# Kernel tuning notes

Hardware: AMD Instinct MI355X
Metric: run time of the kernel (lower is better)

## Reference

```python
import jax, jax.numpy as jnp
import numpy as np

N_DOMAIN = 8
EPS = 1e-05
NUM_FEATURES = 1024
BATCH = 65536


def setup_inputs() -> dict:
    key = jax.random.key(0)
    k1, k2 = jax.random.split(key)
    x = jax.random.normal(k1, (BATCH, NUM_FEATURES), dtype=jnp.float32)
    y = jax.random.randint(k2, (BATCH,), 0, N_DOMAIN, dtype=jnp.int64)
    gamma = jnp.ones((1, NUM_FEATURES), dtype=jnp.float32)
    beta = jnp.zeros((1, NUM_FEATURES), dtype=jnp.float32)
    return {"x": x, "y": y, "gamma": gamma, "beta": beta}


def reference(x, y, gamma, beta):
    # Training-mode domain-specific batchnorm (2D path of DSBatchNorm2).
    y32 = y.astype(jnp.int32)
    ones = jnp.ones((x.shape[0],), dtype=x.dtype)
    count = jax.ops.segment_sum(ones, y32, num_segments=N_DOMAIN)  # [D]
    safe_count = jnp.maximum(count, 1.0)[:, None]                  # [D,1]
    # per-domain mean (biased var, two-pass to match ((x-mean)**2).mean)
    mean = jax.ops.segment_sum(x, y32, num_segments=N_DOMAIN) / safe_count  # [D,F]
    diff = x - mean[y32]                                                    # [N,F]
    var = jax.ops.segment_sum(diff * diff, y32, num_segments=N_DOMAIN) / safe_count
    x_hat = diff / jnp.sqrt(var[y32] + EPS)
    x_norm = gamma * x_hat + beta
    cnt_row = count[y32][:, None]  # [N,1]
    # count>1 -> normalized; count==1 -> raw x; count==0 unreachable
    out = jnp.where(cnt_row > 1.0, x_norm, jnp.where(cnt_row == 1.0, x, 0.0))
    return out
```

## Files before the change

### kernel.cpp

```cpp
#include <hip/hip_runtime.h>


#define BATCH 65536
#define NFEAT 1024
#define NF4   256
#define NDOM  8
#define EPSV  1e-5f

#define WS_SUM   0
#define WS_SQ    8192
#define WS_CNT   16384
#define WS_SCL   16392
#define WS_BIA   24584
#define WS_ZERO_BYTES ((16384 + 8) * 4)

__global__ __launch_bounds__(256) void dsbn_stats(
    const float* __restrict__ x, const int* __restrict__ y,
    float* __restrict__ gsum, float* __restrict__ gsq,
    unsigned* __restrict__ gcnt)
{
  __shared__ float lsum[NDOM][NF4];
  __shared__ float lsq [NDOM][NF4];
  __shared__ unsigned lcnt[NDOM];

  const int tid    = threadIdx.x;
  const int w      = tid >> 6;
  const int lane   = tid & 63;
  const int ftile  = blockIdx.x & 3;
  const int rowgrp = blockIdx.x >> 2;
  const int gw     = rowgrp * 4 + w;
  const int c4     = ftile * 64 + lane;

  for (int j = tid; j < NDOM * NF4; j += 256) {
    (&lsum[0][0])[j] = 0.f;
    (&lsq [0][0])[j] = 0.f;
  }
  if (tid < NDOM) lcnt[tid] = 0u;
  __syncthreads();

  float4 s[NDOM], q[NDOM];
  int cnt[NDOM];
#pragma unroll
  for (int dd = 0; dd < NDOM; ++dd) {
    s[dd] = make_float4(0.f, 0.f, 0.f, 0.f);
    q[dd] = make_float4(0.f, 0.f, 0.f, 0.f);
    cnt[dd] = 0;
  }

  const float4* __restrict__ x4 = reinterpret_cast<const float4*>(x);
  const int r0 = gw * 64;

#define DSBN_ADD(dd, v)                                  \
  { s[dd].x += (v).x; s[dd].y += (v).y;                  \
    s[dd].z += (v).z; s[dd].w += (v).w;                  \
    q[dd].x = fmaf((v).x, (v).x, q[dd].x);               \
    q[dd].y = fmaf((v).y, (v).y, q[dd].y);               \
    q[dd].z = fmaf((v).z, (v).z, q[dd].z);               \
    q[dd].w = fmaf((v).w, (v).w, q[dd].w);               \
    cnt[dd]++; }

#define DSBN_ACC(d, v)                                   \
  switch (d) {                                           \
    case 0: DSBN_ADD(0, v); break;                       \
    case 1: DSBN_ADD(1, v); break;                       \
    case 2: DSBN_ADD(2, v); break;                       \
    case 3: DSBN_ADD(3, v); break;                       \
    case 4: DSBN_ADD(4, v); break;                       \
    case 5: DSBN_ADD(5, v); break;                       \
    case 6: DSBN_ADD(6, v); break;                       \
    default: DSBN_ADD(7, v); break;                      \
  }

#pragma unroll 1
  for (int k = 0; k < 64; k += 4) {
    const int ra = r0 + k;
    float4 va = x4[(size_t)(ra    ) * NF4 + c4];
    float4 vb = x4[(size_t)(ra + 1) * NF4 + c4];
    float4 vc = x4[(size_t)(ra + 2) * NF4 + c4];
    float4 vd = x4[(size_t)(ra + 3) * NF4 + c4];
    int da = __builtin_amdgcn_readfirstlane(y[ra    ]);
    int db = __builtin_amdgcn_readfirstlane(y[ra + 1]);
    int dc = __builtin_amdgcn_readfirstlane(y[ra + 2]);
    int de = __builtin_amdgcn_readfirstlane(y[ra + 3]);
    DSBN_ACC(da, va);
    DSBN_ACC(db, vb);
    DSBN_ACC(dc, vc);
    DSBN_ACC(de, vd);
  }

#pragma unroll
  for (int dd = 0; dd < NDOM; ++dd) {
    const int j0 = lane * 4;
    atomicAdd(&lsum[dd][j0 + 0], s[dd].x);
    atomicAdd(&lsum[dd][j0 + 1], s[dd].y);
    atomicAdd(&lsum[dd][j0 + 2], s[dd].z);
    atomicAdd(&lsum[dd][j0 + 3], s[dd].w);
    atomicAdd(&lsq [dd][j0 + 0], q[dd].x);
    atomicAdd(&lsq [dd][j0 + 1], q[dd].y);
    atomicAdd(&lsq [dd][j0 + 2], q[dd].z);
    atomicAdd(&lsq [dd][j0 + 3], q[dd].w);
  }
  if (ftile == 0 && lane == 0) {
#pragma unroll
    for (int dd = 0; dd < NDOM; ++dd)
      atomicAdd(&lcnt[dd], (unsigned)cnt[dd]);
  }
  __syncthreads();

  for (int i = tid; i < NDOM * NF4; i += 256) {
    const int dd = i >> 8;
    const int j  = i & 255;
    const int fg = dd * NFEAT + ftile * 256 + j;
    atomicAdd(&gsum[fg], lsum[dd][j]);
    atomicAdd(&gsq [fg], lsq [dd][j]);
  }
  if (ftile == 0 && tid < NDOM) atomicAdd(&gcnt[tid], lcnt[tid]);
}

__global__ __launch_bounds__(256) void dsbn_prep(
    const float* __restrict__ gsum, const float* __restrict__ gsq,
    const unsigned* __restrict__ gcnt,
    const float* __restrict__ gamma, const float* __restrict__ beta,
    float* __restrict__ scl, float* __restrict__ bia)
{
  const int i = blockIdx.x * 256 + threadIdx.x;
  const int d = i >> 10;
  const int f = i & 1023;
  const float c    = (float)gcnt[d];
  const float sc   = fmaxf(c, 1.f);
  const float mean = gsum[i] / sc;
  float var = gsq[i] / sc - mean * mean;
  var = fmaxf(var, 0.f);
  float scale, bias;
  if (c > 1.5f) {
    const float inv = 1.f / sqrtf(var + EPSV);
    scale = gamma[f] * inv;
    bias  = fmaf(-mean, scale, beta[f]);
  } else if (c > 0.5f) {
    scale = 1.f; bias = 0.f;
  } else {
    scale = 0.f; bias = 0.f;
  }
  scl[i] = scale;
  bia[i] = bias;
}

__global__ __launch_bounds__(256) void dsbn_norm(
    const float* __restrict__ x, const int* __restrict__ y,
    const float* __restrict__ scl, const float* __restrict__ bia,
    float* __restrict__ out)
{
  const float4* __restrict__ x4 = reinterpret_cast<const float4*>(x);
  const float4* __restrict__ s4 = reinterpret_cast<const float4*>(scl);
  const float4* __restrict__ b4 = reinterpret_cast<const float4*>(bia);
  float4* __restrict__ o4 = reinterpret_cast<float4*>(out);

  const int S = gridDim.x * 256;
  for (int idx = blockIdx.x * 256 + threadIdx.x; idx < BATCH * NF4; idx += S) {
    const int r = idx >> 8;
    const int c = idx & 255;
    const int d = __builtin_amdgcn_readfirstlane(y[r]);
    const float4 v  = x4[idx];
    const float4 sc = s4[d * NF4 + c];
    const float4 bb = b4[d * NF4 + c];
    float4 o;
    o.x = fmaf(v.x, sc.x, bb.x);
    o.y = fmaf(v.y, sc.y, bb.y);
    o.z = fmaf(v.z, sc.z, bb.z);
    o.w = fmaf(v.w, sc.w, bb.w);
    o4[idx] = o;
  }
}

extern "C" void kernel_launch(void* const* d_in, const int* in_sizes, int n_in,
                              void* d_out, int out_size, void* d_ws, size_t ws_size,
                              hipStream_t stream) {
  const float* x     = (const float*)d_in[0];
  const int*   y     = (const int*)  d_in[1];
  const float* gamma = (const float*)d_in[2];
  const float* beta  = (const float*)d_in[3];
  float* out = (float*)d_out;

  float*    ws   = (float*)d_ws;
  float*    gsum = ws + WS_SUM;
  float*    gsq  = ws + WS_SQ;
  unsigned* gcnt = (unsigned*)(ws + WS_CNT);
  float*    scl  = ws + WS_SCL;
  float*    bia  = ws + WS_BIA;

  hipMemsetAsync(ws, 0, WS_ZERO_BYTES, stream);

  dsbn_stats<<<dim3(1024), dim3(256), 0, stream>>>(x, y, gsum, gsq, gcnt);
  dsbn_prep <<<dim3(32),   dim3(256), 0, stream>>>(gsum, gsq, gcnt, gamma, beta, scl, bia);
  dsbn_norm <<<dim3(2048), dim3(256), 0, stream>>>(x, y, scl, bia, out);
}
```

Measured before the change: 612.1 us.

## Sort rows by domain via histogram/scan/scatter and process domain-grouped chunks

```diff
diff --git a/kernel.cpp b/kernel.cpp
--- a/kernel.cpp
+++ b/kernel.cpp
@@ -1,7 +1,7 @@
 #include <hip/hip_runtime.h>
 
 
-#define BATCH 65536
+#define NROW  65536
 #define NFEAT 1024
 #define NF4   256
 #define NDOM  8
@@ -10,111 +10,116 @@
 #define WS_SUM   0
 #define WS_SQ    8192
 #define WS_CNT   16384
-#define WS_SCL   16392
-#define WS_BIA   24584
+#define WS_OFFS  16392
+#define WS_CUR   16401
+#define WS_RIDX  16416
+#define WS_SCL   49184
+#define WS_BIA   57376
 #define WS_ZERO_BYTES ((16384 + 8) * 4)
 
+__global__ __launch_bounds__(256) void dsbn_hist(
+    const int* __restrict__ y, unsigned* __restrict__ gcnt)
+{
+  __shared__ unsigned lh[NDOM];
+  const int tid = threadIdx.x;
+  if (tid < NDOM) lh[tid] = 0u;
+  __syncthreads();
+  const int r = blockIdx.x * 256 + tid;
+  const int d = y[r] & 7;
+  atomicAdd(&lh[d], 1u);
+  __syncthreads();
+  if (tid < NDOM) atomicAdd(&gcnt[tid], lh[tid]);
+}
+
+__global__ void dsbn_scan(const unsigned* __restrict__ gcnt,
+                          unsigned* __restrict__ offs,
+                          unsigned* __restrict__ cursor)
+{
+  if (threadIdx.x == 0) {
+    unsigned c = 0;
+    for (int d = 0; d < NDOM; ++d) { offs[d] = c; cursor[d] = c; c += gcnt[d]; }
+    offs[NDOM] = c;
+  }
+}
+
+__global__ __launch_bounds__(256) void dsbn_scatter(
+    const int* __restrict__ y, unsigned* __restrict__ cursor,
+    unsigned short* __restrict__ ridx)
+{
+  __shared__ unsigned lh[NDOM], lbase[NDOM];
+  const int tid = threadIdx.x;
+  if (tid < NDOM) lh[tid] = 0u;
+  __syncthreads();
+  const int r = blockIdx.x * 256 + tid;
+  const int d = y[r] & 7;
+  const unsigned rank = atomicAdd(&lh[d], 1u);
+  __syncthreads();
+  if (tid < NDOM) lbase[tid] = atomicAdd(&cursor[tid], lh[tid]);
+  __syncthreads();
+  ridx[lbase[d] + rank] = (unsigned short)r;
+}
+
 __global__ __launch_bounds__(256) void dsbn_stats(
-    const float* __restrict__ x, const int* __restrict__ y,
-    float* __restrict__ gsum, float* __restrict__ gsq,
-    unsigned* __restrict__ gcnt)
-{
-  __shared__ float lsum[NDOM][NF4];
-  __shared__ float lsq [NDOM][NF4];
-  __shared__ unsigned lcnt[NDOM];
-
-  const int tid    = threadIdx.x;
-  const int w      = tid >> 6;
-  const int lane   = tid & 63;
-  const int ftile  = blockIdx.x & 3;
-  const int rowgrp = blockIdx.x >> 2;
-  const int gw     = rowgrp * 4 + w;
-  const int c4     = ftile * 64 + lane;
-
-  for (int j = tid; j < NDOM * NF4; j += 256) {
-    (&lsum[0][0])[j] = 0.f;
-    (&lsq [0][0])[j] = 0.f;
-  }
-  if (tid < NDOM) lcnt[tid] = 0u;
-  __syncthreads();
-
-  float4 s[NDOM], q[NDOM];
-  int cnt[NDOM];
+    const float* __restrict__ x, const unsigned short* __restrict__ ridx,
+    const unsigned* __restrict__ offs,
+    float* __restrict__ gsum, float* __restrict__ gsq)
+{
+  const int tid   = threadIdx.x;
+  const int w     = tid >> 6, lane = tid & 63;
+  const int gw    = blockIdx.x * 4 + w;
+  const int chunk = gw >> 2;
+  const int ftile = gw & 3;
+  const int c4    = ftile * 64 + lane;
+  const int p0    = chunk * 32;
+
+  const int myr = (int)ridx[p0 + (lane & 31)];
+
+  int d0 = 0;
 #pragma unroll
-  for (int dd = 0; dd < NDOM; ++dd) {
-    s[dd] = make_float4(0.f, 0.f, 0.f, 0.f);
-    q[dd] = make_float4(0.f, 0.f, 0.f, 0.f);
-    cnt[dd] = 0;
-  }
+  for (int k = 1; k < NDOM; ++k) d0 += (p0 >= (int)offs[k]) ? 1 : 0;
+  const bool single = (p0 + 32 <= (int)offs[d0 + 1]);
 
   const float4* __restrict__ x4 = reinterpret_cast<const float4*>(x);
-  const int r0 = gw * 64;
-
-#define DSBN_ADD(dd, v)                                  \
-  { s[dd].x += (v).x; s[dd].y += (v).y;                  \
-    s[dd].z += (v).z; s[dd].w += (v).w;                  \
-    q[dd].x = fmaf((v).x, (v).x, q[dd].x);               \
-    q[dd].y = fmaf((v).y, (v).y, q[dd].y);               \
-    q[dd].z = fmaf((v).z, (v).z, q[dd].z);               \
-    q[dd].w = fmaf((v).w, (v).w, q[dd].w);               \
-    cnt[dd]++; }
-
-#define DSBN_ACC(d, v)                                   \
-  switch (d) {                                           \
-    case 0: DSBN_ADD(0, v); break;                       \
-    case 1: DSBN_ADD(1, v); break;                       \
-    case 2: DSBN_ADD(2, v); break;                       \
-    case 3: DSBN_ADD(3, v); break;                       \
-    case 4: DSBN_ADD(4, v); break;                       \
-    case 5: DSBN_ADD(5, v); break;                       \
-    case 6: DSBN_ADD(6, v); break;                       \
-    default: DSBN_ADD(7, v); break;                      \
-  }
-
-#pragma unroll 1
-  for (int k = 0; k < 64; k += 4) {
-    const int ra = r0 + k;
-    float4 va = x4[(size_t)(ra    ) * NF4 + c4];
-    float4 vb = x4[(size_t)(ra + 1) * NF4 + c4];
-    float4 vc = x4[(size_t)(ra + 2) * NF4 + c4];
-    float4 vd = x4[(size_t)(ra + 3) * NF4 + c4];
-    int da = __builtin_amdgcn_readfirstlane(y[ra    ]);
-    int db = __builtin_amdgcn_readfirstlane(y[ra + 1]);
-    int dc = __builtin_amdgcn_readfirstlane(y[ra + 2]);
-    int de = __builtin_amdgcn_readfirstlane(y[ra + 3]);
-    DSBN_ACC(da, va);
-    DSBN_ACC(db, vb);
-    DSBN_ACC(dc, vc);
-    DSBN_ACC(de, vd);
-  }
-
-#pragma unroll
-  for (int dd = 0; dd < NDOM; ++dd) {
-    const int j0 = lane * 4;
-    atomicAdd(&lsum[dd][j0 + 0], s[dd].x);
-    atomicAdd(&lsum[dd][j0 + 1], s[dd].y);
-    atomicAdd(&lsum[dd][j0 + 2], s[dd].z);
-    atomicAdd(&lsum[dd][j0 + 3], s[dd].w);
-    atomicAdd(&lsq [dd][j0 + 0], q[dd].x);
-    atomicAdd(&lsq [dd][j0 + 1], q[dd].y);
-    atomicAdd(&lsq [dd][j0 + 2], q[dd].z);
-    atomicAdd(&lsq [dd][j0 + 3], q[dd].w);
-  }
-  if (ftile == 0 && lane == 0) {
-#pragma unroll
-    for (int dd = 0; dd < NDOM; ++dd)
-      atomicAdd(&lcnt[dd], (unsigned)cnt[dd]);
-  }
-  __syncthreads();
-
-  for (int i = tid; i < NDOM * NF4; i += 256) {
-    const int dd = i >> 8;
-    const int j  = i & 255;
-    const int fg = dd * NFEAT + ftile * 256 + j;
-    atomicAdd(&gsum[fg], lsum[dd][j]);
-    atomicAdd(&gsq [fg], lsq [dd][j]);
-  }
-  if (ftile == 0 && tid < NDOM) atomicAdd(&gcnt[tid], lcnt[tid]);
+  float4 s = make_float4(0.f, 0.f, 0.f, 0.f);
+  float4 q = make_float4(0.f, 0.f, 0.f, 0.f);
+
+  auto flush = [&](int dd) {
+    float* gs = gsum + dd * NFEAT + c4 * 4;
+    float* gq = gsq  + dd * NFEAT + c4 * 4;
+    atomicAdd(gs + 0, s.x); atomicAdd(gs + 1, s.y);
+    atomicAdd(gs + 2, s.z); atomicAdd(gs + 3, s.w);
+    atomicAdd(gq + 0, q.x); atomicAdd(gq + 1, q.y);
+    atomicAdd(gq + 2, q.z); atomicAdd(gq + 3, q.w);
+  };
+
+  if (single) {
+#pragma unroll 4
+    for (int k = 0; k < 32; ++k) {
+      const int r = (int)__builtin_amdgcn_readlane((unsigned)myr, (unsigned)k);
+      const float4 v = x4[(size_t)r * NF4 + c4];
+      s.x += v.x; s.y += v.y; s.z += v.z; s.w += v.w;
+      q.x = fmaf(v.x, v.x, q.x); q.y = fmaf(v.y, v.y, q.y);
+      q.z = fmaf(v.z, v.z, q.z); q.w = fmaf(v.w, v.w, q.w);
+    }
+    flush(d0);
+  } else {
+    int d = d0;
+    for (int k = 0; k < 32; ++k) {
+      const int p = p0 + k;
+      const int r = (int)__builtin_amdgcn_readlane((unsigned)myr, (unsigned)k);
+      while (p >= (int)offs[d + 1]) {
+        flush(d);
+        s = make_float4(0.f, 0.f, 0.f, 0.f);
+        q = make_float4(0.f, 0.f, 0.f, 0.f);
+        ++d;
+      }
+      const float4 v = x4[(size_t)r * NF4 + c4];
+      s.x += v.x; s.y += v.y; s.z += v.z; s.w += v.w;
+      q.x = fmaf(v.x, v.x, q.x); q.y = fmaf(v.y, v.y, q.y);
+      q.z = fmaf(v.z, v.z, q.z); q.w = fmaf(v.w, v.w, q.w);
+    }
+    flush(d);
+  }
 }
 
 __global__ __launch_bounds__(256) void dsbn_prep(
@@ -146,29 +151,61 @@
 }
 
 __global__ __launch_bounds__(256) void dsbn_norm(
-    const float* __restrict__ x, const int* __restrict__ y,
+    const float* __restrict__ x, const unsigned short* __restrict__ ridx,
+    const unsigned* __restrict__ offs,
     const float* __restrict__ scl, const float* __restrict__ bia,
     float* __restrict__ out)
 {
+  const int tid   = threadIdx.x;
+  const int w     = tid >> 6, lane = tid & 63;
+  const int gw    = blockIdx.x * 4 + w;
+  const int chunk = gw >> 2;
+  const int ftile = gw & 3;
+  const int c4    = ftile * 64 + lane;
+  const int p0    = chunk * 32;
+
+  const int myr = (int)ridx[p0 + (lane & 31)];
+
+  int d0 = 0;
+#pragma unroll
+  for (int k = 1; k < NDOM; ++k) d0 += (p0 >= (int)offs[k]) ? 1 : 0;
+  const bool single = (p0 + 32 <= (int)offs[d0 + 1]);
+
   const float4* __restrict__ x4 = reinterpret_cast<const float4*>(x);
   const float4* __restrict__ s4 = reinterpret_cast<const float4*>(scl);
   const float4* __restrict__ b4 = reinterpret_cast<const float4*>(bia);
   float4* __restrict__ o4 = reinterpret_cast<float4*>(out);
 
-  const int S = gridDim.x * 256;
-  for (int idx = blockIdx.x * 256 + threadIdx.x; idx < BATCH * NF4; idx += S) {
-    const int r = idx >> 8;
-    const int c = idx & 255;
-    const int d = __builtin_amdgcn_readfirstlane(y[r]);
-    const float4 v  = x4[idx];
-    const float4 sc = s4[d * NF4 + c];
-    const float4 bb = b4[d * NF4 + c];
-    float4 o;
-    o.x = fmaf(v.x, sc.x, bb.x);
-    o.y = fmaf(v.y, sc.y, bb.y);
-    o.z = fmaf(v.z, sc.z, bb.z);
-    o.w = fmaf(v.w, sc.w, bb.w);
-    o4[idx] = o;
+  if (single) {
+    const float4 sc = s4[d0 * NF4 + c4];
+    const float4 bb = b4[d0 * NF4 + c4];
+#pragma unroll 4
+    for (int k = 0; k < 32; ++k) {
+      const int r = (int)__builtin_amdgcn_readlane((unsigned)myr, (unsigned)k);
+      const float4 v = x4[(size_t)r * NF4 + c4];
+      float4 o;
+      o.x = fmaf(v.x, sc.x, bb.x);
+      o.y = fmaf(v.y, sc.y, bb.y);
+      o.z = fmaf(v.z, sc.z, bb.z);
+      o.w = fmaf(v.w, sc.w, bb.w);
+      o4[(size_t)r * NF4 + c4] = o;
+    }
+  } else {
+    int d = d0;
+    for (int k = 0; k < 32; ++k) {
+      const int p = p0 + k;
+      const int r = (int)__builtin_amdgcn_readlane((unsigned)myr, (unsigned)k);
+      while (p >= (int)offs[d + 1]) ++d;
+      const float4 sc = s4[d * NF4 + c4];
+      const float4 bb = b4[d * NF4 + c4];
+      const float4 v = x4[(size_t)r * NF4 + c4];
+      float4 o;
+      o.x = fmaf(v.x, sc.x, bb.x);
+      o.y = fmaf(v.y, sc.y, bb.y);
+      o.z = fmaf(v.z, sc.z, bb.z);
+      o.w = fmaf(v.w, sc.w, bb.w);
+      o4[(size_t)r * NF4 + c4] = o;
+    }
   }
 }
 
@@ -181,16 +218,22 @@
   const float* beta  = (const float*)d_in[3];
   float* out = (float*)d_out;
 
-  float*    ws   = (float*)d_ws;
-  float*    gsum = ws + WS_SUM;
-  float*    gsq  = ws + WS_SQ;
-  unsigned* gcnt = (unsigned*)(ws + WS_CNT);
-  float*    scl  = ws + WS_SCL;
-  float*    bia  = ws + WS_BIA;
+  float*          ws     = (float*)d_ws;
+  float*          gsum   = ws + WS_SUM;
+  float*          gsq    = ws + WS_SQ;
+  unsigned*       gcnt   = (unsigned*)(ws + WS_CNT);
+  unsigned*       offs   = (unsigned*)(ws + WS_OFFS);
+  unsigned*       cursor = (unsigned*)(ws + WS_CUR);
+  unsigned short* ridx   = (unsigned short*)(ws + WS_RIDX);
+  float*          scl    = ws + WS_SCL;
+  float*          bia    = ws + WS_BIA;
 
   hipMemsetAsync(ws, 0, WS_ZERO_BYTES, stream);
 
-  dsbn_stats<<<dim3(1024), dim3(256), 0, stream>>>(x, y, gsum, gsq, gcnt);
-  dsbn_prep <<<dim3(32),   dim3(256), 0, stream>>>(gsum, gsq, gcnt, gamma, beta, scl, bia);
-  dsbn_norm <<<dim3(2048), dim3(256), 0, stream>>>(x, y, scl, bia, out);
-}
+  dsbn_hist   <<<dim3(256),  dim3(256), 0, stream>>>(y, gcnt);
+  dsbn_scan   <<<dim3(1),    dim3(64),  0, stream>>>(gcnt, offs, cursor);
+  dsbn_scatter<<<dim3(256),  dim3(256), 0, stream>>>(y, cursor, ridx);
+  dsbn_stats  <<<dim3(2048), dim3(256), 0, stream>>>(x, ridx, offs, gsum, gsq);
+  dsbn_prep   <<<dim3(32),   dim3(256), 0, stream>>>(gsum, gsq, gcnt, gamma, beta, scl, bia);
+  dsbn_norm   <<<dim3(2048), dim3(256), 0, stream>>>(x, ridx, offs, scl, bia, out);
+}
```

Result: no change. 618.7 us (+1.1%).
